# Kernel optimization log

Hardware: AMD Instinct MI355X
Metric: run time of the kernel (lower is better)

## Reference

```python
import jax, jax.numpy as jnp
import numpy as np

RES = 0.05           # map_resolution_meters
SCENE = 20.0         # scene extent in meters used for input generation
B = 4                # number of batch scenes
N = 8388608          # number of points (2**23)
GRID = int(SCENE / (RES / 2)) + 2          # 802, safe upper bound on rows/cols max
NUM_CELLS = (B + 1) * GRID * GRID + GRID   # static upper bound on flattened index space


def setup_inputs() -> dict:
    key = jax.random.key(0)
    k1, k2, k3 = jax.random.split(key, 3)
    xyz = jax.random.uniform(k1, (N, 3), dtype=jnp.float32) * SCENE
    batch_indices = jax.random.randint(k2, (N,), 0, B, dtype=jnp.int32)
    semantics = jax.random.randint(k3, (N,), 0, 40, dtype=jnp.int32)
    return {"xyz": xyz, "batch_indices": batch_indices, "semantics": semantics}


def _discrete_positive_index(values):
    # values / (res/2), round (half-to-even, matching torch.round), shift to >= 0
    q = jnp.round(values / (RES / 2)).astype(jnp.int32)
    return q - q.min()


def reference(xyz, batch_indices, semantics):
    heights = xyz[:, 1]                       # [N]
    rows = _discrete_positive_index(xyz[:, 2])  # [N] int32
    cols = _discrete_positive_index(xyz[:, 0])  # [N] int32
    rmax = rows.max()
    cmax = cols.max()
    # same (collision-prone) flattening formula as the original module
    flat = batch_indices * (rmax * cmax) + rows * cmax + cols  # [N], < NUM_CELLS

    # scatter_max: per-cell max height
    cell_max = jnp.full((NUM_CELLS,), -jnp.inf, dtype=heights.dtype).at[flat].max(heights)
    is_max = heights == cell_max[flat]
    # argmax per cell: smallest point index achieving the cell max (deterministic tiebreak)
    idx = jnp.arange(N, dtype=jnp.int32)
    cell_arg = jnp.full((NUM_CELLS,), N, dtype=jnp.int32).at[flat].min(jnp.where(is_max, idx, N))
    keep = idx == cell_arg[flat]              # [N] bool: point survives filtering

    kept_heights = jnp.where(keep, heights, jnp.float32(0.0))
    return kept_heights, keep
```

## Files before the change

### kernel.cpp

```cpp
#include <hip/hip_runtime.h>
#include <climits>

static constexpr int kN = 8388608;
static constexpr int kNumCells = 3216822;
static constexpr int kMaxFlat = 2560800;
static constexpr int kNBk = (kMaxFlat >> 12) + 1;
static constexpr int kCap = 16384;
static constexpr int kChunk = 4096;
static constexpr int kB = 512;

typedef float __attribute__((ext_vector_type(4))) f32x4;
typedef int   __attribute__((ext_vector_type(4))) i32x4;

__device__ __align__(16) unsigned long long g_keyb[(unsigned)kNBk * kCap];
__device__ __align__(16) unsigned short g_cellb[(unsigned)kNBk * kCap];
__device__ unsigned g_cursor[kNBk * 16];
__device__ unsigned long long g_cell[kNumCells];
__device__ int g_minr = INT_MAX, g_maxr = INT_MIN;
__device__ int g_minc = INT_MAX, g_maxc = INT_MIN;
__device__ int g_fb = 0;

__device__ __forceinline__ int quant(float v) {
    return (int)rintf(v * 40.0f);
}
__device__ __forceinline__ bool okfast() {
    return g_minr == 0 && g_maxr == 800 && g_minc == 0 && g_maxc == 800;
}

__global__ void k_cursor() {
    int i = blockIdx.x * blockDim.x + threadIdx.x;
    if (i < kNBk) g_cursor[i << 4] = (unsigned)(i * kCap);
}

__global__ void __launch_bounds__(512) k_main(const float* __restrict__ xyz,
                                              const int* __restrict__ bidx, int n,
                                              float* __restrict__ out, int total,
                                              int zb) {
    const int tid = threadIdx.x;
    if (blockIdx.x < zb) {
        int t = blockIdx.x * blockDim.x + tid;
        int S = zb * blockDim.x;
        float4 f4 = make_float4(0.f, 0.f, 0.f, 0.f);
        float4* o4 = (float4*)out;
        const int no4 = total >> 2;
        for (int i = t; i < no4; i += S) o4[i] = f4;
        for (int i = (no4 << 2) + t; i < total; i += S) out[i] = 0.f;
        return;
    }
    const int chunk0 = (blockIdx.x - zb) * kChunk;
    if (chunk0 >= n) return;

    __shared__ unsigned s_cnt[kNBk];
    __shared__ unsigned s_scan[kNBk];
    __shared__ unsigned long long s_key[kChunk];
    __shared__ unsigned s_cb[kChunk];
    int* s_mm = (int*)s_key;
    unsigned* s_wsum = ((unsigned*)s_key) + 32;
    for (int i = tid; i < kNBk; i += kB) s_cnt[i] = 0;
    __syncthreads();

    unsigned hb[8], flu[8], rank[8];
    bool val[8];
    int mnr = INT_MAX, mxr = INT_MIN, mnc = INT_MAX, mxc = INT_MIN;
    const f32x4* p = (const f32x4*)xyz;
    const i32x4* bp = (const i32x4*)bidx;
    const int g0 = (chunk0 >> 2) + tid;
#pragma unroll
    for (int k = 0; k < 2; ++k) {
        const int gidx = g0 + (k << 9);
        const int pbase = gidx << 2;
        float xs[4], hs[4], zs[4]; int bs[4];
        if (pbase + 3 < n) {
            f32x4 f0 = p[3 * gidx + 0];
            f32x4 f1 = p[3 * gidx + 1];
            f32x4 f2 = p[3 * gidx + 2];
            i32x4 b4 = bp[gidx];
            xs[0]=f0.x; hs[0]=f0.y; zs[0]=f0.z;
            xs[1]=f0.w; hs[1]=f1.x; zs[1]=f1.y;
            xs[2]=f1.z; hs[2]=f1.w; zs[2]=f2.x;
            xs[3]=f2.y; hs[3]=f2.z; zs[3]=f2.w;
            bs[0]=b4.x; bs[1]=b4.y; bs[2]=b4.z; bs[3]=b4.w;
        } else {
#pragma unroll
            for (int j = 0; j < 4; ++j) {
                int i = pbase + j;
                bool v = i < n;
                xs[j] = v ? xyz[3 * i + 0] : 0.f;
                hs[j] = v ? xyz[3 * i + 1] : 0.f;
                zs[j] = v ? xyz[3 * i + 2] : 0.f;
                bs[j] = v ? bidx[i] : 0;
            }
        }
#pragma unroll
        for (int j = 0; j < 4; ++j) {
            const int e = (k << 2) + j;
            bool v = (pbase + j) < n;
            val[e] = v;
            int qr = quant(zs[j]);
            int qc = quant(xs[j]);
            if (v) {
                mnr = min(mnr, qr); mxr = max(mxr, qr);
                mnc = min(mnc, qc); mxc = max(mxc, qc);
            }
            long long fl = (long long)bs[j] * 640000 + (long long)qr * 800 + qc;
            unsigned f = (unsigned)min(max(fl, 0LL), (long long)kMaxFlat);
            flu[e] = f;
            hb[e] = __float_as_uint(hs[j]);
            rank[e] = v ? (unsigned)atomicAdd(&s_cnt[f >> 12], 1u) : 0u;
        }
    }
#pragma unroll
    for (int off = 32; off > 0; off >>= 1) {
        mnr = min(mnr, __shfl_down(mnr, off));
        mxr = max(mxr, __shfl_down(mxr, off));
        mnc = min(mnc, __shfl_down(mnc, off));
        mxc = max(mxc, __shfl_down(mxc, off));
    }
    const int w = tid >> 6, lane = tid & 63;
    if (lane == 0) {
        s_mm[w * 4 + 0] = mnr; s_mm[w * 4 + 1] = mxr;
        s_mm[w * 4 + 2] = mnc; s_mm[w * 4 + 3] = mxc;
    }
    __syncthreads();
    if (tid == 0) {
        int a0 = INT_MAX, a1 = INT_MIN, a2 = INT_MAX, a3 = INT_MIN;
#pragma unroll
        for (int i = 0; i < 8; ++i) {
            a0 = min(a0, s_mm[i * 4 + 0]); a1 = max(a1, s_mm[i * 4 + 1]);
            a2 = min(a2, s_mm[i * 4 + 2]); a3 = max(a3, s_mm[i * 4 + 3]);
        }
        atomicMin(&g_minr, a0); atomicMax(&g_maxr, a1);
        atomicMin(&g_minc, a2); atomicMax(&g_maxc, a3);
    }
    int e0 = tid * 2;
    unsigned l0 = (e0 + 0 < kNBk) ? s_cnt[e0 + 0] : 0u;
    unsigned l1 = (e0 + 1 < kNBk) ? s_cnt[e0 + 1] : 0u;
    unsigned tsum = l0 + l1;
    unsigned inc = tsum;
#pragma unroll
    for (int off = 1; off < 64; off <<= 1) {
        unsigned v = __shfl_up(inc, off);
        if (lane >= off) inc += v;
    }
    if (lane == 63) s_wsum[w] = inc;
    __syncthreads();
    if (tid == 0) {
        unsigned a = 0;
#pragma unroll
        for (int i = 0; i < 8; ++i) { unsigned t = s_wsum[i]; s_wsum[i] = a; a += t; }
    }
    __syncthreads();
    unsigned excl = inc - tsum + s_wsum[w];
    if (e0 + 0 < kNBk) s_scan[e0 + 0] = excl;
    if (e0 + 1 < kNBk) s_scan[e0 + 1] = excl + l0;
    __syncthreads();
    for (int i = tid; i < kNBk; i += kB) {
        unsigned c = s_cnt[i];
        if (c) {
            unsigned pos = atomicAdd(&g_cursor[i << 4], c);
            if (pos + c > (unsigned)((i + 1) * kCap)) { g_fb = 1; s_cnt[i] = 0u; }
            else s_cnt[i] = pos - s_scan[i];
        }
    }
#pragma unroll
    for (int e = 0; e < 8; ++e) {
        if (val[e]) {
            const int k = e >> 2, j = e & 3;
            unsigned idx = (unsigned)(((g0 + (k << 9)) << 2) + j);
            unsigned pos = s_scan[flu[e] >> 12] + rank[e];
            s_key[pos] = ((unsigned long long)hb[e] << 32) | idx;
            s_cb[pos] = flu[e];
        }
    }
    __syncthreads();
    const int nstaged = min(n - chunk0, kChunk);
    for (int i = tid; i < nstaged; i += kB) {
        unsigned cb = s_cb[i];
        unsigned bkt = cb >> 12;
        unsigned dst = s_cnt[bkt] + (unsigned)i;
        g_keyb[dst] = s_key[i];
        g_cellb[dst] = (unsigned short)(cb & 4095u);
    }
}

__global__ void __launch_bounds__(256) k_reduce(int n, float* __restrict__ out) {
    if (g_fb || !okfast()) return;
    __shared__ unsigned s_hmax[4096], s_imin[4096];
    const int tid = threadIdx.x;
    const int bk = blockIdx.x;
    for (int i = tid; i < 4096; i += 256) { s_hmax[i] = 0u; s_imin[i] = 0xFFFFFFFFu; }
    __syncthreads();
    const unsigned lo = (unsigned)(bk * kCap);
    unsigned hi = g_cursor[bk << 4];
    const unsigned cap = (unsigned)((bk + 1) * kCap);
    if (hi > cap) hi = cap;
    for (unsigned i = lo + tid; i < hi; i += 256)
        atomicMax(&s_hmax[g_cellb[i]], (unsigned)(g_keyb[i] >> 32));
    __syncthreads();
    for (unsigned i = lo + tid; i < hi; i += 256) {
        unsigned long long k = g_keyb[i];
        unsigned c = g_cellb[i];
        if ((unsigned)(k >> 32) == s_hmax[c])
            atomicMin(&s_imin[c], (unsigned)k);
    }
    __syncthreads();
    for (int c = tid; c < 4096; c += 256) {
        unsigned im = s_imin[c];
        if (im != 0xFFFFFFFFu) {
            out[im] = __uint_as_float(s_hmax[c]);
            out[n + im] = 1.0f;
        }
    }
}

__global__ void k_fb_zero() {
    if (!g_fb && okfast()) return;
    int i = blockIdx.x * blockDim.x + threadIdx.x;
    int stride = gridDim.x * blockDim.x;
    for (int c = i; c < kNumCells; c += stride) g_cell[c] = 0ULL;
}
__global__ void k_fb_scatter(const float* __restrict__ xyz,
                             const int* __restrict__ bidx, int n) {
    if (!g_fb && okfast()) return;
    const int minr = g_minr, minc = g_minc;
    const int rmax = g_maxr - minr, cmax = g_maxc - minc;
    int t = blockIdx.x * blockDim.x + threadIdx.x;
    int S = gridDim.x * blockDim.x;
    for (int i = t; i < n; i += S) {
        float x = xyz[3 * i + 0], h = xyz[3 * i + 1], z = xyz[3 * i + 2];
        int qr = quant(z) - minr, qc = quant(x) - minc;
        int flat = bidx[i] * (rmax * cmax) + qr * cmax + qc;
        if (flat >= 0 && flat < kNumCells) {
            unsigned long long key =
                ((unsigned long long)__float_as_uint(h) << 32) | (unsigned)(~i);
            if (key > g_cell[flat]) atomicMax(&g_cell[flat], key);
        }
    }
}
__global__ void k_fb_fin(int n, float* __restrict__ out) {
    if (!g_fb && okfast()) return;
    int i = blockIdx.x * blockDim.x + threadIdx.x;
    int stride = gridDim.x * blockDim.x;
    for (int c = i; c < kNumCells; c += stride) {
        unsigned long long key = g_cell[c];
        if (key == 0ULL) continue;
        unsigned winner = ~(unsigned)key;
        out[winner] = __uint_as_float((unsigned)(key >> 32));
        out[n + winner] = 1.0f;
    }
}
__global__ void k_reset() {
    if (threadIdx.x == 0 && blockIdx.x == 0) {
        g_fb = 0;
        g_minr = INT_MAX; g_maxr = INT_MIN;
        g_minc = INT_MAX; g_maxc = INT_MIN;
    }
}

extern "C" void kernel_launch(void* const* d_in, const int* in_sizes, int n_in,
                              void* d_out, int out_size, void* d_ws, size_t ws_size,
                              hipStream_t stream) {
    const float* xyz = (const float*)d_in[0];
    const int* bidx = (const int*)d_in[1];
    int n = in_sizes[1];

    const int zb = 256;
    int gridMain = zb + (n + kChunk - 1) / kChunk;
    k_cursor<<<(kNBk + 255) / 256, 256, 0, stream>>>();
    k_main<<<gridMain, kB, 0, stream>>>(xyz, bidx, n, (float*)d_out, out_size, zb);
    k_reduce<<<kNBk, 256, 0, stream>>>(n, (float*)d_out);
    k_fb_zero<<<2048, 256, 0, stream>>>();
    k_fb_scatter<<<4096, 256, 0, stream>>>(xyz, bidx, n);
    k_fb_fin<<<2048, 256, 0, stream>>>(n, (float*)d_out);
    k_reset<<<1, 64, 0, stream>>>();
}
```

Baseline: 242.5 us.

## Pack height and inverted index into one 64-bit key for single-pass reduce

The point index in each staged key is stored bit-inverted, so a single 64-bit shared-memory atomicMax per point yields both the max height and the smallest index among ties. This replaces the two-pass max-then-min reduction and halves the global reads of the bucket buffers. Bucket cursors are now relative counts that k_reduce resets to zero after reading, which removes the separate cursor-init kernel launch. The cost is 64-bit shared atomics, and the design relies on cursors being zero on the very first call, which holds because globals are zero-initialised.

```diff
diff --git a/kernel.cpp b/kernel.cpp
--- a/kernel.cpp
+++ b/kernel.cpp
@@ -25,11 +25,6 @@
 }
 __device__ __forceinline__ bool okfast() {
     return g_minr == 0 && g_maxr == 800 && g_minc == 0 && g_maxc == 800;
-}
-
-__global__ void k_cursor() {
-    int i = blockIdx.x * blockDim.x + threadIdx.x;
-    if (i < kNBk) g_cursor[i << 4] = (unsigned)(i * kCap);
 }
 
 __global__ void __launch_bounds__(512) k_main(const float* __restrict__ xyz,
@@ -158,8 +153,8 @@
         unsigned c = s_cnt[i];
         if (c) {
             unsigned pos = atomicAdd(&g_cursor[i << 4], c);
-            if (pos + c > (unsigned)((i + 1) * kCap)) { g_fb = 1; s_cnt[i] = 0u; }
-            else s_cnt[i] = pos - s_scan[i];
+            if (pos + c > (unsigned)kCap) { g_fb = 1; s_cnt[i] = 0u; }
+            else s_cnt[i] = (unsigned)(i * kCap) + pos - s_scan[i];
         }
     }
 #pragma unroll
@@ -168,7 +163,7 @@
             const int k = e >> 2, j = e & 3;
             unsigned idx = (unsigned)(((g0 + (k << 9)) << 2) + j);
             unsigned pos = s_scan[flu[e] >> 12] + rank[e];
-            s_key[pos] = ((unsigned long long)hb[e] << 32) | idx;
+            s_key[pos] = ((unsigned long long)hb[e] << 32) | (unsigned)(~idx);
             s_cb[pos] = flu[e];
         }
     }
@@ -184,30 +179,26 @@
 }
 
 __global__ void __launch_bounds__(256) k_reduce(int n, float* __restrict__ out) {
-    if (g_fb || !okfast()) return;
-    __shared__ unsigned s_hmax[4096], s_imin[4096];
     const int tid = threadIdx.x;
     const int bk = blockIdx.x;
-    for (int i = tid; i < 4096; i += 256) { s_hmax[i] = 0u; s_imin[i] = 0xFFFFFFFFu; }
+    unsigned cnt = g_cursor[bk << 4];
+    if (cnt > (unsigned)kCap) cnt = (unsigned)kCap;
+    __syncthreads();
+    if (tid == 0) g_cursor[bk << 4] = 0u;
+    if (g_fb || !okfast()) return;
+    __shared__ unsigned long long s_cw[4096];
+    for (int i = tid; i < 4096; i += 256) s_cw[i] = 0ULL;
     __syncthreads();
     const unsigned lo = (unsigned)(bk * kCap);
-    unsigned hi = g_cursor[bk << 4];
-    const unsigned cap = (unsigned)((bk + 1) * kCap);
-    if (hi > cap) hi = cap;
+    const unsigned hi = lo + cnt;
     for (unsigned i = lo + tid; i < hi; i += 256)
-        atomicMax(&s_hmax[g_cellb[i]], (unsigned)(g_keyb[i] >> 32));
-    __syncthreads();
-    for (unsigned i = lo + tid; i < hi; i += 256) {
-        unsigned long long k = g_keyb[i];
-        unsigned c = g_cellb[i];
-        if ((unsigned)(k >> 32) == s_hmax[c])
-            atomicMin(&s_imin[c], (unsigned)k);
-    }
+        atomicMax(&s_cw[g_cellb[i]], g_keyb[i]);
     __syncthreads();
     for (int c = tid; c < 4096; c += 256) {
-        unsigned im = s_imin[c];
-        if (im != 0xFFFFFFFFu) {
-            out[im] = __uint_as_float(s_hmax[c]);
+        unsigned long long v = s_cw[c];
+        if (v != 0ULL) {
+            unsigned im = ~(unsigned)v;
+            out[im] = __uint_as_float((unsigned)(v >> 32));
             out[n + im] = 1.0f;
         }
     }
@@ -266,7 +257,6 @@
 
     const int zb = 256;
     int gridMain = zb + (n + kChunk - 1) / kChunk;
-    k_cursor<<<(kNBk + 255) / 256, 256, 0, stream>>>();
     k_main<<<gridMain, kB, 0, stream>>>(xyz, bidx, n, (float*)d_out, out_size, zb);
     k_reduce<<<kNBk, 256, 0, stream>>>(n, (float*)d_out);
     k_fb_zero<<<2048, 256, 0, stream>>>();
```

Measured after the change: 236.0 us. 2.7% less time.
